# Optimization experiments

Hardware: AMD Instinct MI355X
Metric: run time of the kernel (lower is better)

## Reference

```python
import jax, jax.numpy as jnp
import numpy as np

B, S, DIM = 2, 2048, 1024
H, W = 16, 256
HD = DIM // H
SCALE = HD ** -0.5


def setup_inputs() -> dict:
    key = jax.random.key(0)
    ks = jax.random.split(key, 9)
    std = DIM ** -0.5
    return {
        "x": jax.random.normal(ks[0], (B, S, DIM), dtype=jnp.float32),
        "Wq": jax.random.normal(ks[1], (DIM, DIM), dtype=jnp.float32) * std,
        "bq": jnp.zeros((DIM,), dtype=jnp.float32),
        "Wk": jax.random.normal(ks[2], (DIM, DIM), dtype=jnp.float32) * std,
        "bk": jnp.zeros((DIM,), dtype=jnp.float32),
        "Wv": jax.random.normal(ks[3], (DIM, DIM), dtype=jnp.float32) * std,
        "bv": jnp.zeros((DIM,), dtype=jnp.float32),
        "Wo": jax.random.normal(ks[4], (DIM, DIM), dtype=jnp.float32) * std,
        "bo": jnp.zeros((DIM,), dtype=jnp.float32),
    }


def reference(x, Wq, bq, Wk, bk, Wv, bv, Wo, bo):
    b, s, dim = x.shape
    q = (x @ Wq + bq).reshape(b, s, H, HD).transpose(0, 2, 1, 3)  # [B,H,S,HD]
    k = (x @ Wk + bk).reshape(b, s, H, HD).transpose(0, 2, 1, 3)
    v = (x @ Wv + bv).reshape(b, s, H, HD).transpose(0, 2, 1, 3)

    scores = jnp.einsum("bhid,bhjd->bhij", q, k) * SCALE  # [B,H,S,S]
    i = jnp.arange(s)[:, None]
    j = jnp.arange(s)[None, :]
    # valid keys: within causal sliding window [i-W+1, i]
    valid = (j <= i) & (j >= i - W + 1)
    scores = jnp.where(valid, scores, -jnp.inf)
    attn = jax.nn.softmax(scores, axis=-1)
    out = jnp.einsum("bhij,bhjd->bhid", attn, v)  # [B,H,S,HD]
    out = out.transpose(0, 2, 1, 3).reshape(b, s, dim)
    return out @ Wo + bo
```

## Files before the change

kernel.cpp:

```cpp
#include <hip/hip_runtime.h>
#include <stdint.h>

typedef __bf16 bf16;
typedef __bf16 bf16x8 __attribute__((ext_vector_type(8)));
typedef float f32x4 __attribute__((ext_vector_type(4)));

#define MFMA16(a, b, c) __builtin_amdgcn_mfma_f32_16x16x32_bf16((a), (b), (c), 0, 0, 0)

__device__ __forceinline__ void ldsdma16(const void* g, void* l) {
  __builtin_amdgcn_global_load_lds((const __attribute__((address_space(1))) void*)g,
                                   (__attribute__((address_space(3))) void*)l, 16, 0, 0);
}

__global__ __launch_bounds__(256) void prep_kernel(const float* __restrict__ x,
                                                   const float* __restrict__ Wq,
                                                   const float* __restrict__ Wk,
                                                   const float* __restrict__ Wv,
                                                   const float* __restrict__ Wo,
                                                   bf16* __restrict__ WT,
                                                   bf16* __restrict__ xb) {
  if (blockIdx.z == 4) {
    const int t = (blockIdx.y * 16 + blockIdx.x) * 256 + threadIdx.x;
#pragma unroll
    for (int it = 0; it < 16; ++it) {
      const int idx = (it * 65536 + t) * 4;
      float4 v = *(const float4*)(x + idx);
      union { bf16 h[4]; uint2 u; } p;
      p.h[0] = (bf16)v.x; p.h[1] = (bf16)v.y; p.h[2] = (bf16)v.z; p.h[3] = (bf16)v.w;
      *(uint2*)(xb + idx) = p.u;
    }
    return;
  }
  __shared__ float tile[64][65];
  const float* src = blockIdx.z == 0 ? Wq : blockIdx.z == 1 ? Wk : blockIdx.z == 2 ? Wv : Wo;
  bf16* dst = WT + (size_t)blockIdx.z * 1024 * 1024;
  const int k0 = blockIdx.y * 64, n0 = blockIdx.x * 64;
  const int rr = threadIdx.x >> 6, c = threadIdx.x & 63;
#pragma unroll
  for (int i = 0; i < 16; ++i) {
    int r = i * 4 + rr;
    tile[r][c] = src[(size_t)(k0 + r) * 1024 + n0 + c];
  }
  __syncthreads();
#pragma unroll
  for (int i = 0; i < 16; ++i) {
    int r = i * 4 + rr;
    dst[(size_t)(n0 + r) * 1024 + k0 + c] = (bf16)tile[c][r];
  }
}

__device__ __forceinline__ void gemm_mainloop(const bf16* __restrict__ A,
                                              const bf16* __restrict__ BT, int K,
                                              int m0, int n0, bf16* As, bf16* Bs,
                                              f32x4 acc[4][4]) {
  const int tid = threadIdx.x;
  const int lane = tid & 63;
  const int wave = tid >> 6;
  const int wm = wave >> 1, wn = wave & 1;
  const int quad = lane >> 4, l16 = lane & 15;

  const f32x4 zero = {0.f, 0.f, 0.f, 0.f};
#pragma unroll
  for (int i = 0; i < 4; ++i)
#pragma unroll
    for (int j = 0; j < 4; ++j) acc[i][j] = zero;

  const int ch0 = wave * 128 + lane;

  for (int k0 = 0; k0 < K; k0 += 32) {
#pragma unroll
    for (int c = 0; c < 2; ++c) {
      int chunk = ch0 + c * 64;
      int row = chunk >> 2;
      int cg = (chunk & 3) ^ ((row >> 1) & 3);
      ldsdma16(A + (size_t)(m0 + row) * K + k0 + cg * 8,
               (char*)As + (size_t)(wave * 128 + c * 64) * 16);
      ldsdma16(BT + (size_t)(n0 + row) * K + k0 + cg * 8,
               (char*)Bs + (size_t)(wave * 128 + c * 64) * 16);
    }
    __syncthreads();
    bf16x8 af[4], bfv[4];
#pragma unroll
    for (int i = 0; i < 4; ++i) {
      int ra = wm * 64 + i * 16 + l16;
      af[i] = ((const bf16x8*)As)[ra * 4 + (quad ^ ((ra >> 1) & 3))];
      int rb = wn * 64 + i * 16 + l16;
      bfv[i] = ((const bf16x8*)Bs)[rb * 4 + (quad ^ ((rb >> 1) & 3))];
    }
#pragma unroll
    for (int i = 0; i < 4; ++i)
#pragma unroll
      for (int j = 0; j < 4; ++j) acc[i][j] = MFMA16(af[i], bfv[j], acc[i][j]);
    __syncthreads();
  }
}

__global__ __launch_bounds__(256) void qkv_gemm(const bf16* __restrict__ xb,
                                                const bf16* __restrict__ WT,
                                                const float* __restrict__ bq,
                                                const float* __restrict__ bk,
                                                const float* __restrict__ bv,
                                                bf16* __restrict__ Qd,
                                                bf16* __restrict__ Kd,
                                                bf16* __restrict__ Vt) {
  __shared__ bf16 As[128 * 32] __attribute__((aligned(16)));
  __shared__ bf16 Bs[128 * 32] __attribute__((aligned(16)));
  f32x4 acc[4][4];
  const int m0 = blockIdx.y * 128, n0 = blockIdx.x * 128;
  gemm_mainloop(xb, WT, 1024, m0, n0, As, Bs, acc);

  const int lane = threadIdx.x & 63, wave = threadIdx.x >> 6;
  const int wm = wave >> 1, wn = wave & 1;
  const int quad = lane >> 4, l16 = lane & 15;
#pragma unroll
  for (int j = 0; j < 4; ++j) {
    const int n = n0 + wn * 64 + j * 16 + l16;
    const int sel = n >> 10, d = n & 1023;
    const float bias = (sel == 0 ? bq : sel == 1 ? bk : bv)[d];
    const float scl = (sel == 0) ? 0.125f : 1.f;
    const int h = d >> 6, hd = d & 63;
#pragma unroll
    for (int i = 0; i < 4; ++i) {
#pragma unroll
      for (int r = 0; r < 4; ++r) {
        const int token = m0 + wm * 64 + i * 16 + quad * 4 + r;
        const int bb = token >> 11, s = token & 2047;
        const float v = (acc[i][j][r] + bias) * scl;
        if (sel == 2) {
          Vt[((((size_t)bb * 16 + h) * 64 + hd) << 11) + s] = (bf16)v;
        } else {
          bf16* dst = (sel == 0) ? Qd : Kd;
          dst[((((size_t)bb * 16 + h) * 2048 + s) << 6) + hd] = (bf16)v;
        }
      }
    }
  }
}

__global__ __launch_bounds__(256) void attn_kernel(const bf16* __restrict__ Q,
                                                   const bf16* __restrict__ K,
                                                   const bf16* __restrict__ Vt,
                                                   bf16* __restrict__ Ao) {
  __shared__ bf16 Ps[4][16 * 72] __attribute__((aligned(16)));

  const int tid = threadIdx.x, lane = tid & 63, wave = tid >> 6;
  const int quad = lane >> 4, l16 = lane & 15;
  const int qt = blockIdx.x, h = blockIdx.y, b = blockIdx.z;
  const int q0 = qt * 64;
  const size_t base = ((size_t)(b * 16 + h)) * 2048 * 64;
  const bf16* Qb = Q + base + (size_t)q0 * 64;
  const bf16* Kb = K + base;
  const bf16* Vb = Vt + base;

  const int qrow = wave * 16 + l16;
  const bf16x8 qa0 = *(const bf16x8*)(Qb + (size_t)qrow * 64 + quad * 8);
  const bf16x8 qa1 = *(const bf16x8*)(Qb + (size_t)qrow * 64 + 32 + quad * 8);

  float lrow[4];
  f32x4 oacc[4];
  const f32x4 zero = {0.f, 0.f, 0.f, 0.f};
#pragma unroll
  for (int r = 0; r < 4; ++r) lrow[r] = 0.f;
#pragma unroll
  for (int t = 0; t < 4; ++t) oacc[t] = zero;

  const int clo = (qt >= 4) ? (qt - 4) : 0;
  for (int ck = clo; ck <= qt; ++ck) {
    const int c0 = ck * 64;

    f32x4 sc[4];
#pragma unroll
    for (int nt = 0; nt < 4; ++nt) {
      const bf16* kp = Kb + (size_t)(c0 + nt * 16 + l16) * 64 + quad * 8;
      bf16x8 kb0 = *(const bf16x8*)kp;
      bf16x8 kb1 = *(const bf16x8*)(kp + 32);
      f32x4 s = MFMA16(qa0, kb0, zero);
      sc[nt] = MFMA16(qa1, kb1, s);
    }

    if (ck == qt) {
#pragma unroll
      for (int r = 0; r < 4; ++r) {
        const int i = q0 + wave * 16 + quad * 4 + r;
#pragma unroll
        for (int nt = 0; nt < 4; ++nt) {
          const int j = c0 + nt * 16 + l16;
          const float p = (j <= i) ? __expf(sc[nt][r]) : 0.f;
          sc[nt][r] = p;
          lrow[r] += p;
        }
      }
    } else if (qt >= 4 && ck == qt - 4) {
#pragma unroll
      for (int r = 0; r < 4; ++r) {
        const int i = q0 + wave * 16 + quad * 4 + r;
#pragma unroll
        for (int nt = 0; nt < 4; ++nt) {
          const int j = c0 + nt * 16 + l16;
          const float p = (j + 255 >= i) ? __expf(sc[nt][r]) : 0.f;
          sc[nt][r] = p;
          lrow[r] += p;
        }
      }
    } else {
#pragma unroll
      for (int r = 0; r < 4; ++r) {
#pragma unroll
        for (int nt = 0; nt < 4; ++nt) {
          const float p = __expf(sc[nt][r]);
          sc[nt][r] = p;
          lrow[r] += p;
        }
      }
    }

#pragma unroll
    for (int nt = 0; nt < 4; ++nt)
#pragma unroll
      for (int r = 0; r < 4; ++r)
        Ps[wave][(quad * 4 + r) * 72 + nt * 16 + l16] = (bf16)sc[nt][r];
    asm volatile("s_waitcnt lgkmcnt(0)" ::: "memory");
    bf16x8 pa0 = ((const bf16x8*)Ps[wave])[l16 * 9 + quad];
    bf16x8 pa1 = ((const bf16x8*)Ps[wave])[l16 * 9 + 4 + quad];

#pragma unroll
    for (int ht = 0; ht < 4; ++ht) {
      const bf16* vp = Vb + (size_t)(ht * 16 + l16) * 2048 + c0 + quad * 8;
      bf16x8 vb0 = *(const bf16x8*)vp;
      bf16x8 vb1 = *(const bf16x8*)(vp + 32);
      f32x4 o = MFMA16(pa0, vb0, oacc[ht]);
      oacc[ht] = MFMA16(pa1, vb1, o);
    }
  }

#pragma unroll
  for (int r = 0; r < 4; ++r) {
#pragma unroll
    for (int m = 8; m >= 1; m >>= 1) lrow[r] += __shfl_xor(lrow[r], m, 64);
    const float inv = 1.f / lrow[r];
    const int row = q0 + wave * 16 + quad * 4 + r;
    const size_t outb = ((size_t)(b * 2048 + row)) * 1024 + h * 64;
#pragma unroll
    for (int ht = 0; ht < 4; ++ht)
      Ao[outb + ht * 16 + l16] = (bf16)(oacc[ht][r] * inv);
  }
}

__global__ __launch_bounds__(256) void out_gemm(const bf16* __restrict__ Ain,
                                                const bf16* __restrict__ WoT,
                                                const float* __restrict__ bo,
                                                float* __restrict__ out) {
  __shared__ bf16 As[128 * 32] __attribute__((aligned(16)));
  __shared__ bf16 Bs[64 * 32] __attribute__((aligned(16)));
  const int tid = threadIdx.x, lane = tid & 63, wave = tid >> 6;
  const int wm = wave >> 1, wn = wave & 1;
  const int quad = lane >> 4, l16 = lane & 15;
  const int m0 = blockIdx.y * 128, n0 = blockIdx.x * 64;

  f32x4 acc[4][2];
  const f32x4 zero = {0.f, 0.f, 0.f, 0.f};
#pragma unroll
  for (int i = 0; i < 4; ++i)
#pragma unroll
    for (int j = 0; j < 2; ++j) acc[i][j] = zero;

  for (int k0 = 0; k0 < 1024; k0 += 32) {
#pragma unroll
    for (int c = 0; c < 2; ++c) {
      int chunk = wave * 64 + c * 256 + lane;
      int row = chunk >> 2;
      int cg = (chunk & 3) ^ ((row >> 1) & 3);
      ldsdma16(Ain + (size_t)(m0 + row) * 1024 + k0 + cg * 8,
               (char*)As + (size_t)(wave * 64 + c * 256) * 16);
    }
    {
      int chunk = wave * 64 + lane;
      int row = chunk >> 2;
      int cg = (chunk & 3) ^ ((row >> 1) & 3);
      ldsdma16(WoT + (size_t)(n0 + row) * 1024 + k0 + cg * 8,
               (char*)Bs + (size_t)(wave * 64) * 16);
    }
    __syncthreads();
    bf16x8 af[4], bfv[2];
#pragma unroll
    for (int i = 0; i < 4; ++i) {
      int ra = wm * 64 + i * 16 + l16;
      af[i] = ((const bf16x8*)As)[ra * 4 + (quad ^ ((ra >> 1) & 3))];
    }
#pragma unroll
    for (int j = 0; j < 2; ++j) {
      int rb = wn * 32 + j * 16 + l16;
      bfv[j] = ((const bf16x8*)Bs)[rb * 4 + (quad ^ ((rb >> 1) & 3))];
    }
#pragma unroll
    for (int i = 0; i < 4; ++i)
#pragma unroll
      for (int j = 0; j < 2; ++j) acc[i][j] = MFMA16(af[i], bfv[j], acc[i][j]);
    __syncthreads();
  }

#pragma unroll
  for (int j = 0; j < 2; ++j) {
    const int n = n0 + wn * 32 + j * 16 + l16;
    const float bias = bo[n];
#pragma unroll
    for (int i = 0; i < 4; ++i) {
#pragma unroll
      for (int r = 0; r < 4; ++r) {
        const int token = m0 + wm * 64 + i * 16 + quad * 4 + r;
        out[(size_t)token * 1024 + n] = acc[i][j][r] + bias;
      }
    }
  }
}

extern "C" void kernel_launch(void* const* d_in, const int* in_sizes, int n_in,
                              void* d_out, int out_size, void* d_ws, size_t ws_size,
                              hipStream_t stream) {
  const float* x  = (const float*)d_in[0];
  const float* Wq = (const float*)d_in[1];
  const float* bq = (const float*)d_in[2];
  const float* Wk = (const float*)d_in[3];
  const float* bk = (const float*)d_in[4];
  const float* Wv = (const float*)d_in[5];
  const float* bv = (const float*)d_in[6];
  const float* Wo = (const float*)d_in[7];
  const float* bo = (const float*)d_in[8];
  float* out = (float*)d_out;

  char* ws = (char*)d_ws;
  bf16* xb = (bf16*)(ws);
  bf16* WT = (bf16*)(ws + ((size_t)8 << 20));
  bf16* Qd = (bf16*)(ws + ((size_t)16 << 20));
  bf16* Kd = (bf16*)(ws + ((size_t)24 << 20));
  bf16* Vt = (bf16*)(ws + ((size_t)32 << 20));
  bf16* Ao = (bf16*)(ws + ((size_t)40 << 20));

  prep_kernel<<<dim3(16, 16, 5), 256, 0, stream>>>(x, Wq, Wk, Wv, Wo, WT, xb);
  qkv_gemm<<<dim3(24, 32), 256, 0, stream>>>(xb, WT, bq, bk, bv, Qd, Kd, Vt);
  attn_kernel<<<dim3(32, 16, 2), 256, 0, stream>>>(Qd, Kd, Vt, Ao);
  out_gemm<<<dim3(16, 32), 256, 0, stream>>>(Ao, WT + (size_t)3 * 1024 * 1024, bo, out);
}
```

Before: 190.4 us.

## Write QKV contiguously, add V transpose kernel, widen GEMM K-tile, use exp2

The QKV GEMM now writes one token-major [tokens,3072] buffer with coalesced stores instead of scattered per-head and transposed writes. A separate kernel transposes V through LDS. Attention reads Q and K from the combined buffer, loads V before the softmax so the loads can overlap it, and uses exp2 with the log2e factor folded into the Q scale. Both GEMMs double the K tile to 64 with an 8-way XOR swizzle, which halves the barrier count. The cost is an extra kernel launch and an extra round trip through memory for V, plus strided Q/K reads inside attention.

```diff
diff --git a/kernel.cpp b/kernel.cpp
--- a/kernel.cpp
+++ b/kernel.cpp
@@ -49,96 +49,98 @@
   }
 }
 
-__device__ __forceinline__ void gemm_mainloop(const bf16* __restrict__ A,
-                                              const bf16* __restrict__ BT, int K,
-                                              int m0, int n0, bf16* As, bf16* Bs,
-                                              f32x4 acc[4][4]) {
-  const int tid = threadIdx.x;
-  const int lane = tid & 63;
-  const int wave = tid >> 6;
-  const int wm = wave >> 1, wn = wave & 1;
-  const int quad = lane >> 4, l16 = lane & 15;
-
-  const f32x4 zero = {0.f, 0.f, 0.f, 0.f};
-#pragma unroll
-  for (int i = 0; i < 4; ++i)
-#pragma unroll
-    for (int j = 0; j < 4; ++j) acc[i][j] = zero;
-
-  const int ch0 = wave * 128 + lane;
-
-  for (int k0 = 0; k0 < K; k0 += 32) {
-#pragma unroll
-    for (int c = 0; c < 2; ++c) {
-      int chunk = ch0 + c * 64;
-      int row = chunk >> 2;
-      int cg = (chunk & 3) ^ ((row >> 1) & 3);
-      ldsdma16(A + (size_t)(m0 + row) * K + k0 + cg * 8,
-               (char*)As + (size_t)(wave * 128 + c * 64) * 16);
-      ldsdma16(BT + (size_t)(n0 + row) * K + k0 + cg * 8,
-               (char*)Bs + (size_t)(wave * 128 + c * 64) * 16);
-    }
-    __syncthreads();
-    bf16x8 af[4], bfv[4];
-#pragma unroll
-    for (int i = 0; i < 4; ++i) {
-      int ra = wm * 64 + i * 16 + l16;
-      af[i] = ((const bf16x8*)As)[ra * 4 + (quad ^ ((ra >> 1) & 3))];
-      int rb = wn * 64 + i * 16 + l16;
-      bfv[i] = ((const bf16x8*)Bs)[rb * 4 + (quad ^ ((rb >> 1) & 3))];
-    }
-#pragma unroll
-    for (int i = 0; i < 4; ++i)
-#pragma unroll
-      for (int j = 0; j < 4; ++j) acc[i][j] = MFMA16(af[i], bfv[j], acc[i][j]);
-    __syncthreads();
-  }
-}
-
 __global__ __launch_bounds__(256) void qkv_gemm(const bf16* __restrict__ xb,
                                                 const bf16* __restrict__ WT,
                                                 const float* __restrict__ bq,
                                                 const float* __restrict__ bk,
                                                 const float* __restrict__ bv,
-                                                bf16* __restrict__ Qd,
-                                                bf16* __restrict__ Kd,
-                                                bf16* __restrict__ Vt) {
-  __shared__ bf16 As[128 * 32] __attribute__((aligned(16)));
-  __shared__ bf16 Bs[128 * 32] __attribute__((aligned(16)));
-  f32x4 acc[4][4];
-  const int m0 = blockIdx.y * 128, n0 = blockIdx.x * 128;
-  gemm_mainloop(xb, WT, 1024, m0, n0, As, Bs, acc);
-
-  const int lane = threadIdx.x & 63, wave = threadIdx.x >> 6;
+                                                bf16* __restrict__ QKVc) {
+  __shared__ bf16 As[128 * 64] __attribute__((aligned(16)));
+  __shared__ bf16 Bs[128 * 64] __attribute__((aligned(16)));
+  const int tid = threadIdx.x, lane = tid & 63, wave = tid >> 6;
   const int wm = wave >> 1, wn = wave & 1;
   const int quad = lane >> 4, l16 = lane & 15;
+  const int m0 = blockIdx.y * 128, n0 = blockIdx.x * 128;
+
+  f32x4 acc[4][4];
+  const f32x4 zero = {0.f, 0.f, 0.f, 0.f};
+#pragma unroll
+  for (int i = 0; i < 4; ++i)
+#pragma unroll
+    for (int j = 0; j < 4; ++j) acc[i][j] = zero;
+
+  for (int k0 = 0; k0 < 1024; k0 += 64) {
+#pragma unroll
+    for (int b2 = 0; b2 < 4; ++b2) {
+      int chunk = wave * 256 + b2 * 64 + lane;
+      int row = chunk >> 3;
+      int cg = (chunk & 7) ^ (row & 7);
+      ldsdma16(xb + (size_t)(m0 + row) * 1024 + k0 + cg * 8,
+               (char*)As + (size_t)(wave * 256 + b2 * 64) * 16);
+      ldsdma16(WT + (size_t)(n0 + row) * 1024 + k0 + cg * 8,
+               (char*)Bs + (size_t)(wave * 256 + b2 * 64) * 16);
+    }
+    __syncthreads();
+#pragma unroll
+    for (int s = 0; s < 2; ++s) {
+      bf16x8 af[4], bfv[4];
+#pragma unroll
+      for (int i = 0; i < 4; ++i) {
+        int ra = wm * 64 + i * 16 + l16;
+        af[i] = ((const bf16x8*)As)[ra * 8 + ((s * 4 + quad) ^ (ra & 7))];
+        int rb = wn * 64 + i * 16 + l16;
+        bfv[i] = ((const bf16x8*)Bs)[rb * 8 + ((s * 4 + quad) ^ (rb & 7))];
+      }
+#pragma unroll
+      for (int i = 0; i < 4; ++i)
+#pragma unroll
+        for (int j = 0; j < 4; ++j) acc[i][j] = MFMA16(af[i], bfv[j], acc[i][j]);
+    }
+    __syncthreads();
+  }
+
+  const int sel = blockIdx.x >> 3;
+  const float* bp = sel == 0 ? bq : sel == 1 ? bk : bv;
+  const float scl = (sel == 0) ? 0.18033688f : 1.f;
 #pragma unroll
   for (int j = 0; j < 4; ++j) {
     const int n = n0 + wn * 64 + j * 16 + l16;
-    const int sel = n >> 10, d = n & 1023;
-    const float bias = (sel == 0 ? bq : sel == 1 ? bk : bv)[d];
-    const float scl = (sel == 0) ? 0.125f : 1.f;
-    const int h = d >> 6, hd = d & 63;
+    const float bias = bp[n & 1023];
 #pragma unroll
     for (int i = 0; i < 4; ++i) {
 #pragma unroll
       for (int r = 0; r < 4; ++r) {
         const int token = m0 + wm * 64 + i * 16 + quad * 4 + r;
-        const int bb = token >> 11, s = token & 2047;
-        const float v = (acc[i][j][r] + bias) * scl;
-        if (sel == 2) {
-          Vt[((((size_t)bb * 16 + h) * 64 + hd) << 11) + s] = (bf16)v;
-        } else {
-          bf16* dst = (sel == 0) ? Qd : Kd;
-          dst[((((size_t)bb * 16 + h) * 2048 + s) << 6) + hd] = (bf16)v;
-        }
-      }
-    }
-  }
-}
-
-__global__ __launch_bounds__(256) void attn_kernel(const bf16* __restrict__ Q,
-                                                   const bf16* __restrict__ K,
+        QKVc[(size_t)token * 3072 + n] = (bf16)((acc[i][j][r] + bias) * scl);
+      }
+    }
+  }
+}
+
+__global__ __launch_bounds__(256) void v_transpose(const bf16* __restrict__ QKVc,
+                                                   bf16* __restrict__ Vt) {
+  __shared__ bf16 tile[64][72] __attribute__((aligned(16)));
+  const int tid = threadIdx.x;
+  const int st = blockIdx.x, h = blockIdx.y, b = blockIdx.z;
+  {
+    const int t = tid >> 2, cg = (tid & 3) * 16;
+    const bf16* src = QKVc + ((size_t)(b * 2048 + st * 64 + t)) * 3072 + 2048 + h * 64 + cg;
+    bf16x8 v0 = *(const bf16x8*)src;
+    bf16x8 v1 = *(const bf16x8*)(src + 8);
+    *(bf16x8*)&tile[t][cg] = v0;
+    *(bf16x8*)&tile[t][cg + 8] = v1;
+  }
+  __syncthreads();
+  const int hd = tid & 63, sg = (tid >> 6) * 16;
+  bf16 o[16];
+#pragma unroll
+  for (int i = 0; i < 16; ++i) o[i] = tile[sg + i][hd];
+  bf16* dst = Vt + ((size_t)((b * 16 + h) * 64 + hd)) * 2048 + st * 64 + sg;
+  *(bf16x8*)dst = *(bf16x8*)&o[0];
+  *(bf16x8*)(dst + 8) = *(bf16x8*)&o[8];
+}
+
+__global__ __launch_bounds__(256) void attn_kernel(const bf16* __restrict__ QKVc,
                                                    const bf16* __restrict__ Vt,
                                                    bf16* __restrict__ Ao) {
   __shared__ bf16 Ps[4][16 * 72] __attribute__((aligned(16)));
@@ -147,14 +149,12 @@
   const int quad = lane >> 4, l16 = lane & 15;
   const int qt = blockIdx.x, h = blockIdx.y, b = blockIdx.z;
   const int q0 = qt * 64;
-  const size_t base = ((size_t)(b * 16 + h)) * 2048 * 64;
-  const bf16* Qb = Q + base + (size_t)q0 * 64;
-  const bf16* Kb = K + base;
-  const bf16* Vb = Vt + base;
+  const bf16* Vb = Vt + ((size_t)(b * 16 + h)) * 2048 * 64;
 
   const int qrow = wave * 16 + l16;
-  const bf16x8 qa0 = *(const bf16x8*)(Qb + (size_t)qrow * 64 + quad * 8);
-  const bf16x8 qa1 = *(const bf16x8*)(Qb + (size_t)qrow * 64 + 32 + quad * 8);
+  const bf16* qp = QKVc + (size_t)(b * 2048 + q0 + qrow) * 3072 + h * 64 + quad * 8;
+  const bf16x8 qa0 = *(const bf16x8*)qp;
+  const bf16x8 qa1 = *(const bf16x8*)(qp + 32);
 
   float lrow[4];
   f32x4 oacc[4];
@@ -171,13 +171,21 @@
     f32x4 sc[4];
 #pragma unroll
     for (int nt = 0; nt < 4; ++nt) {
-      const bf16* kp = Kb + (size_t)(c0 + nt * 16 + l16) * 64 + quad * 8;
+      const bf16* kp = QKVc + (size_t)(b * 2048 + c0 + nt * 16 + l16) * 3072 + 1024 + h * 64 + quad * 8;
       bf16x8 kb0 = *(const bf16x8*)kp;
       bf16x8 kb1 = *(const bf16x8*)(kp + 32);
       f32x4 s = MFMA16(qa0, kb0, zero);
       sc[nt] = MFMA16(qa1, kb1, s);
     }
 
+    bf16x8 vb0[4], vb1[4];
+#pragma unroll
+    for (int ht = 0; ht < 4; ++ht) {
+      const bf16* vp = Vb + (size_t)(ht * 16 + l16) * 2048 + c0 + quad * 8;
+      vb0[ht] = *(const bf16x8*)vp;
+      vb1[ht] = *(const bf16x8*)(vp + 32);
+    }
+
     if (ck == qt) {
 #pragma unroll
       for (int r = 0; r < 4; ++r) {
@@ -185,7 +193,7 @@
 #pragma unroll
         for (int nt = 0; nt < 4; ++nt) {
           const int j = c0 + nt * 16 + l16;
-          const float p = (j <= i) ? __expf(sc[nt][r]) : 0.f;
+          const float p = (j <= i) ? exp2f(sc[nt][r]) : 0.f;
           sc[nt][r] = p;
           lrow[r] += p;
         }
@@ -197,7 +205,7 @@
 #pragma unroll
         for (int nt = 0; nt < 4; ++nt) {
           const int j = c0 + nt * 16 + l16;
-          const float p = (j + 255 >= i) ? __expf(sc[nt][r]) : 0.f;
+          const float p = (j + 255 >= i) ? exp2f(sc[nt][r]) : 0.f;
           sc[nt][r] = p;
           lrow[r] += p;
         }
@@ -207,7 +215,7 @@
       for (int r = 0; r < 4; ++r) {
 #pragma unroll
         for (int nt = 0; nt < 4; ++nt) {
-          const float p = __expf(sc[nt][r]);
+          const float p = exp2f(sc[nt][r]);
           sc[nt][r] = p;
           lrow[r] += p;
         }
@@ -225,11 +233,8 @@
 
 #pragma unroll
     for (int ht = 0; ht < 4; ++ht) {
-      const bf16* vp = Vb + (size_t)(ht * 16 + l16) * 2048 + c0 + quad * 8;
-      bf16x8 vb0 = *(const bf16x8*)vp;
-      bf16x8 vb1 = *(const bf16x8*)(vp + 32);
-      f32x4 o = MFMA16(pa0, vb0, oacc[ht]);
-      oacc[ht] = MFMA16(pa1, vb1, o);
+      f32x4 o = MFMA16(pa0, vb0[ht], oacc[ht]);
+      oacc[ht] = MFMA16(pa1, vb1[ht], o);
     }
   }
 
@@ -250,8 +255,8 @@
                                                 const bf16* __restrict__ WoT,
                                                 const float* __restrict__ bo,
                                                 float* __restrict__ out) {
-  __shared__ bf16 As[128 * 32] __attribute__((aligned(16)));
-  __shared__ bf16 Bs[64 * 32] __attribute__((aligned(16)));
+  __shared__ bf16 As[128 * 64] __attribute__((aligned(16)));
+  __shared__ bf16 Bs[64 * 64] __attribute__((aligned(16)));
   const int tid = threadIdx.x, lane = tid & 63, wave = tid >> 6;
   const int wm = wave >> 1, wn = wave & 1;
   const int quad = lane >> 4, l16 = lane & 15;
@@ -264,38 +269,42 @@
 #pragma unroll
     for (int j = 0; j < 2; ++j) acc[i][j] = zero;
 
-  for (int k0 = 0; k0 < 1024; k0 += 32) {
-#pragma unroll
-    for (int c = 0; c < 2; ++c) {
-      int chunk = wave * 64 + c * 256 + lane;
-      int row = chunk >> 2;
-      int cg = (chunk & 3) ^ ((row >> 1) & 3);
+  for (int k0 = 0; k0 < 1024; k0 += 64) {
+#pragma unroll
+    for (int b2 = 0; b2 < 4; ++b2) {
+      int chunk = wave * 256 + b2 * 64 + lane;
+      int row = chunk >> 3;
+      int cg = (chunk & 7) ^ (row & 7);
       ldsdma16(Ain + (size_t)(m0 + row) * 1024 + k0 + cg * 8,
-               (char*)As + (size_t)(wave * 64 + c * 256) * 16);
-    }
-    {
-      int chunk = wave * 64 + lane;
-      int row = chunk >> 2;
-      int cg = (chunk & 3) ^ ((row >> 1) & 3);
+               (char*)As + (size_t)(wave * 256 + b2 * 64) * 16);
+    }
+#pragma unroll
+    for (int b2 = 0; b2 < 2; ++b2) {
+      int chunk = wave * 128 + b2 * 64 + lane;
+      int row = chunk >> 3;
+      int cg = (chunk & 7) ^ (row & 7);
       ldsdma16(WoT + (size_t)(n0 + row) * 1024 + k0 + cg * 8,
-               (char*)Bs + (size_t)(wave * 64) * 16);
+               (char*)Bs + (size_t)(wave * 128 + b2 * 64) * 16);
     }
     __syncthreads();
-    bf16x8 af[4], bfv[2];
-#pragma unroll
-    for (int i = 0; i < 4; ++i) {
-      int ra = wm * 64 + i * 16 + l16;
-      af[i] = ((const bf16x8*)As)[ra * 4 + (quad ^ ((ra >> 1) & 3))];
-    }
-#pragma unroll
-    for (int j = 0; j < 2; ++j) {
-      int rb = wn * 32 + j * 16 + l16;
-      bfv[j] = ((const bf16x8*)Bs)[rb * 4 + (quad ^ ((rb >> 1) & 3))];
-    }
-#pragma unroll
-    for (int i = 0; i < 4; ++i)
-#pragma unroll
-      for (int j = 0; j < 2; ++j) acc[i][j] = MFMA16(af[i], bfv[j], acc[i][j]);
+#pragma unroll
+    for (int s = 0; s < 2; ++s) {
+      bf16x8 af[4], bfv[2];
+#pragma unroll
+      for (int i = 0; i < 4; ++i) {
+        int ra = wm * 64 + i * 16 + l16;
+        af[i] = ((const bf16x8*)As)[ra * 8 + ((s * 4 + quad) ^ (ra & 7))];
+      }
+#pragma unroll
+      for (int j = 0; j < 2; ++j) {
+        int rb = wn * 32 + j * 16 + l16;
+        bfv[j] = ((const bf16x8*)Bs)[rb * 8 + ((s * 4 + quad) ^ (rb & 7))];
+      }
+#pragma unroll
+      for (int i = 0; i < 4; ++i)
+#pragma unroll
+        for (int j = 0; j < 2; ++j) acc[i][j] = MFMA16(af[i], bfv[j], acc[i][j]);
+    }
     __syncthreads();
   }
 
@@ -329,15 +338,15 @@
   float* out = (float*)d_out;
 
   char* ws = (char*)d_ws;
-  bf16* xb = (bf16*)(ws);
-  bf16* WT = (bf16*)(ws + ((size_t)8 << 20));
-  bf16* Qd = (bf16*)(ws + ((size_t)16 << 20));
-  bf16* Kd = (bf16*)(ws + ((size_t)24 << 20));
-  bf16* Vt = (bf16*)(ws + ((size_t)32 << 20));
-  bf16* Ao = (bf16*)(ws + ((size_t)40 << 20));
+  bf16* xb   = (bf16*)(ws);
+  bf16* WT   = (bf16*)(ws + ((size_t)8 << 20));
+  bf16* QKVc = (bf16*)(ws + ((size_t)16 << 20));
+  bf16* Vt   = (bf16*)(ws + ((size_t)40 << 20));
+  bf16* Ao   = (bf16*)(ws + ((size_t)48 << 20));
 
   prep_kernel<<<dim3(16, 16, 5), 256, 0, stream>>>(x, Wq, Wk, Wv, Wo, WT, xb);
-  qkv_gemm<<<dim3(24, 32), 256, 0, stream>>>(xb, WT, bq, bk, bv, Qd, Kd, Vt);
-  attn_kernel<<<dim3(32, 16, 2), 256, 0, stream>>>(Qd, Kd, Vt, Ao);
+  qkv_gemm<<<dim3(24, 32), 256, 0, stream>>>(xb, WT, bq, bk, bv, QKVc);
+  v_transpose<<<dim3(32, 16, 2), 256, 0, stream>>>(QKVc, Vt);
+  attn_kernel<<<dim3(32, 16, 2), 256, 0, stream>>>(QKVc, Vt, Ao);
   out_gemm<<<dim3(16, 32), 256, 0, stream>>>(Ao, WT + (size_t)3 * 1024 * 1024, bo, out);
 }
```

Result: no change. 193.3 us (+1.5%).
